# Optimization experiments

Measured on AMD Instinct MI355X. Metric: run time of the kernel, lower is better.

Reference implementation:

```python
import jax, jax.numpy as jnp
import numpy as np

D_MODEL = 1024
NUM_HEADS = 16

def setup_inputs() -> dict:
    key = jax.random.key(0)
    ks = jax.random.split(key, 5)
    std = np.sqrt(2.0 / (D_MODEL + D_MODEL))
    def w(k):
        # trunc_normal approx: normal clipped to +-3 std
        v = jax.random.truncated_normal(k, -3.0, 3.0, (D_MODEL, D_MODEL), dtype=jnp.float32) * std
        return v
    return {
        "x": jax.random.normal(ks[0], (2, 2048, D_MODEL), dtype=jnp.float32),
        "w_q": w(ks[1]),
        "w_k": w(ks[2]),
        "w_v": w(ks[3]),
        "w_o": w(ks[4]),
    }

def reference(x, w_q, w_k, w_v, w_o):
    B, S, D = x.shape
    H = NUM_HEADS
    dk = D // H
    # Linear: y = x @ W^T  (weight is [d_out, d_in])
    def proj(w):
        y = jnp.einsum('bsd,ed->bse', x, w)
        return y.reshape(B, S, H, dk).transpose(0, 2, 1, 3)  # [B,H,S,dk]
    q, k, v = proj(w_q), proj(w_k), proj(w_v)
    scale = 1.0 / jnp.sqrt(jnp.float32(dk))
    scores = jnp.einsum('bhqd,bhkd->bhqk', q, k) * scale  # [B,H,S,S]
    causal = jnp.tril(jnp.ones((S, S), dtype=bool))
    scores = jnp.where(causal, scores, -jnp.inf)
    attn = jax.nn.softmax(scores, axis=-1)
    out = jnp.einsum('bhqk,bhkd->bhqd', attn, v)  # [B,H,S,dk]
    out = out.transpose(0, 2, 1, 3).reshape(B, S, D)
    return jnp.einsum('bsd,ed->bse', out, w_o)
```

## Files before the change

### kernel.cpp

```cpp
#include <hip/hip_runtime.h>
#include <hip/hip_bf16.h>
#include <stdint.h>

#define S_LEN 2048
#define DM    1024
#define NH    16
#define DK    64
#define NBATCH 2

typedef __attribute__((ext_vector_type(8))) short bf8_t;
typedef __attribute__((ext_vector_type(4))) short s4_t;
typedef __attribute__((ext_vector_type(4))) float f4_t;

using bf16 = __hip_bfloat16;

#define NEG_BIG (-1.0e30f)
#define SCALE2  (0.125f * 1.44269504088896f)

static __device__ __forceinline__ f4_t mfma16(bf8_t a, bf8_t b, f4_t c) {
    return __builtin_amdgcn_mfma_f32_16x16x32_bf16(a, b, c, 0, 0, 0);
}

static __device__ __forceinline__ short f2b(float f) {
    __hip_bfloat16 h = __float2bfloat16(f);
    return *reinterpret_cast<short*>(&h);
}

static __device__ __forceinline__ void g2l16(const bf16* g, bf16* l) {
#if __has_builtin(__builtin_amdgcn_global_load_lds)
    __builtin_amdgcn_global_load_lds(
        (const __attribute__((address_space(1))) void*)g,
        (__attribute__((address_space(3))) void*)l, 16, 0, 0);
#else
    *(bf8_t*)l = *(const bf8_t*)g;
#endif
}

__global__ __launch_bounds__(256)
void cvt_all(const float* __restrict__ x,  const float* __restrict__ wq,
             const float* __restrict__ wk, const float* __restrict__ wv,
             const float* __restrict__ wo, bf16* __restrict__ ob) {
    const size_t SEG = 1u << 20;
    size_t i = ((size_t)blockIdx.x * 256 + threadIdx.x) * 8;
    const float* src;
    if      (i < 4 * SEG) src = x  + i;
    else if (i < 5 * SEG) src = wq + (i - 4 * SEG);
    else if (i < 6 * SEG) src = wk + (i - 5 * SEG);
    else if (i < 7 * SEG) src = wv + (i - 6 * SEG);
    else                  src = wo + (i - 7 * SEG);
    float4 f0 = *(const float4*)(src);
    float4 f1 = *(const float4*)(src + 4);
    bf8_t v;
    v[0]=f2b(f0.x); v[1]=f2b(f0.y); v[2]=f2b(f0.z); v[3]=f2b(f0.w);
    v[4]=f2b(f1.x); v[5]=f2b(f1.y); v[6]=f2b(f1.z); v[7]=f2b(f1.w);
    *(bf8_t*)(ob + i) = v;
}

#define GEMM_B_MAINLOOP(Aptr, Bptr)                                          \
    __shared__ bf16 As[128][32];                                             \
    __shared__ bf16 Bs[128][32];                                             \
    const int tid  = threadIdx.x;                                            \
    const int lane = tid & 63;                                               \
    const int w    = tid >> 6;                                               \
    const int wr   = w >> 1, wc = w & 1;                                     \
    const int lhi  = lane >> 4, llo = lane & 15;                             \
    const int bm   = blockIdx.x * 128;                                       \
    const int bn   = blockIdx.y * 128;                                       \
    const int r0c  = tid >> 2;                           \
    const int c0c  = (tid & 3) << 3;                     \
    const int r1c  = (256 + tid) >> 2;                                       \
    f4_t acc[4][4] = {};                                                     \
    for (int k0 = 0; k0 < 1024; k0 += 32) {                                  \
        __syncthreads();                                                     \
        g2l16(Aptr + (size_t)(bm + r0c) * 1024 + k0 + c0c,                   \
              &As[0][0] + (size_t)tid * 8);                                  \
        g2l16(Aptr + (size_t)(bm + r1c) * 1024 + k0 + c0c,                   \
              &As[0][0] + (size_t)(256 + tid) * 8);                          \
        g2l16(Bptr + (size_t)(bn + r0c) * 1024 + k0 + c0c,                   \
              &Bs[0][0] + (size_t)tid * 8);                                  \
        g2l16(Bptr + (size_t)(bn + r1c) * 1024 + k0 + c0c,                   \
              &Bs[0][0] + (size_t)(256 + tid) * 8);                          \
        asm volatile("s_waitcnt vmcnt(0)" ::: "memory");                     \
        __syncthreads();                                                     \
        bf8_t af[4], bfr[4];                                                 \
        _Pragma("unroll")                                                    \
        for (int i = 0; i < 4; ++i) {                                        \
            af[i]  = *(const bf8_t*)(&As[wr * 64 + i * 16 + llo][lhi * 8]);  \
            bfr[i] = *(const bf8_t*)(&Bs[wc * 64 + i * 16 + llo][lhi * 8]);  \
        }                                                                    \
        _Pragma("unroll")                                                    \
        for (int mi = 0; mi < 4; ++mi)                                       \
            _Pragma("unroll")                                                \
            for (int ni = 0; ni < 4; ++ni)                                   \
                acc[mi][ni] = mfma16(af[mi], bfr[ni], acc[mi][ni]);          \
    }

__global__ __launch_bounds__(256)
void gemm_qkv_b(const bf16* __restrict__ xb,
                const bf16* __restrict__ wqb, const bf16* __restrict__ wkb,
                const bf16* __restrict__ wvb,
                bf16* __restrict__ qws, bf16* __restrict__ kws,
                bf16* __restrict__ vtws) {
    const int z = blockIdx.z;
    const bf16* Wb = (z == 0) ? wqb : (z == 1) ? wkb : wvb;
    GEMM_B_MAINLOOP(xb, Wb)

    if (z < 2) {
        bf16* C = z ? kws : qws;
        const float sc = z ? 1.0f : SCALE2;
        #pragma unroll
        for (int mi = 0; mi < 4; ++mi)
            #pragma unroll
            for (int ni = 0; ni < 4; ++ni)
                #pragma unroll
                for (int r = 0; r < 4; ++r) {
                    int m = bm + wr * 64 + mi * 16 + lhi * 4 + r;
                    int n = bn + wc * 64 + ni * 16 + llo;
                    int b = m >> 11, s = m & (S_LEN - 1);
                    int h = n >> 6,  d = n & (DK - 1);
                    C[(((size_t)(b * NH + h) * S_LEN) + s) * DK + d] =
                        __float2bfloat16(acc[mi][ni][r] * sc);
                }
    } else {
        #pragma unroll
        for (int mi = 0; mi < 4; ++mi)
            #pragma unroll
            for (int ni = 0; ni < 4; ++ni) {
                int m0 = bm + wr * 64 + mi * 16 + lhi * 4;
                int n  = bn + wc * 64 + ni * 16 + llo;
                int b = m0 >> 11, s0 = m0 & (S_LEN - 1);
                int h = n >> 6,   d  = n & (DK - 1);
                s4_t pk;
                #pragma unroll
                for (int r = 0; r < 4; ++r) pk[r] = f2b(acc[mi][ni][r]);
                *(s4_t*)&vtws[(((size_t)(b * NH + h) * DK) + d) * S_LEN + s0] = pk;
            }
    }
}

__global__ __launch_bounds__(256)
void gemm_o_b(const bf16* __restrict__ A, const bf16* __restrict__ Wb,
              float* __restrict__ C) {
    GEMM_B_MAINLOOP(A, Wb)
    #pragma unroll
    for (int mi = 0; mi < 4; ++mi)
        #pragma unroll
        for (int ni = 0; ni < 4; ++ni)
            #pragma unroll
            for (int r = 0; r < 4; ++r) {
                int m = bm + wr * 64 + mi * 16 + lhi * 4 + r;
                int n = bn + wc * 64 + ni * 16 + llo;
                C[(size_t)m * DM + n] = acc[mi][ni][r];
            }
}

__global__ __launch_bounds__(256)
void gemm_qkv_f32(const float* __restrict__ x,
                  const float* __restrict__ wqp, const float* __restrict__ wkp,
                  const float* __restrict__ wvp,
                  bf16* __restrict__ qws, bf16* __restrict__ kws,
                  bf16* __restrict__ vtws) {
    constexpr int K = DM;
    constexpr int BM = 128, BK = 32, LDT = BK + 8;
    const int z = blockIdx.z;
    const float* W = (z == 0) ? wqp : (z == 1) ? wkp : wvp;
    __shared__ bf16 As[BM][LDT];
    __shared__ bf16 Bs[BM][LDT];
    const int tid  = threadIdx.x;
    const int lane = tid & 63;
    const int w    = tid >> 6;
    const int wr   = w >> 1, wc = w & 1;
    const int lhi  = lane >> 4, llo = lane & 15;
    const int bm   = blockIdx.x * BM;
    const int bn   = blockIdx.y * BM;
    f4_t acc[4][4] = {};
    for (int k0 = 0; k0 < K; k0 += BK) {
        __syncthreads();
        #pragma unroll
        for (int t = 0; t < 2; ++t) {
            int c   = t * 256 + tid;
            int row = c >> 2;
            int col = (c & 3) << 3;
            {
                const float* s0 = x + (size_t)(bm + row) * K + k0 + col;
                float4 f0 = *(const float4*)(s0);
                float4 f1 = *(const float4*)(s0 + 4);
                bf8_t a8;
                a8[0]=f2b(f0.x); a8[1]=f2b(f0.y); a8[2]=f2b(f0.z); a8[3]=f2b(f0.w);
                a8[4]=f2b(f1.x); a8[5]=f2b(f1.y); a8[6]=f2b(f1.z); a8[7]=f2b(f1.w);
                *(bf8_t*)(&As[row][col]) = a8;
            }
            {
                const float* s0 = W + (size_t)(bn + row) * K + k0 + col;
                float4 f0 = *(const float4*)(s0);
                float4 f1 = *(const float4*)(s0 + 4);
                bf8_t b8;
                b8[0]=f2b(f0.x); b8[1]=f2b(f0.y); b8[2]=f2b(f0.z); b8[3]=f2b(f0.w);
                b8[4]=f2b(f1.x); b8[5]=f2b(f1.y); b8[6]=f2b(f1.z); b8[7]=f2b(f1.w);
                *(bf8_t*)(&Bs[row][col]) = b8;
            }
        }
        __syncthreads();
        bf8_t af[4], bfr[4];
        #pragma unroll
        for (int i = 0; i < 4; ++i) {
            af[i]  = *(const bf8_t*)(&As[wr * 64 + i * 16 + llo][lhi * 8]);
            bfr[i] = *(const bf8_t*)(&Bs[wc * 64 + i * 16 + llo][lhi * 8]);
        }
        #pragma unroll
        for (int mi = 0; mi < 4; ++mi)
            #pragma unroll
            for (int ni = 0; ni < 4; ++ni)
                acc[mi][ni] = mfma16(af[mi], bfr[ni], acc[mi][ni]);
    }
    if (z < 2) {
        bf16* C = z ? kws : qws;
        const float sc = z ? 1.0f : SCALE2;
        #pragma unroll
        for (int mi = 0; mi < 4; ++mi)
            #pragma unroll
            for (int ni = 0; ni < 4; ++ni)
                #pragma unroll
                for (int r = 0; r < 4; ++r) {
                    int m = bm + wr * 64 + mi * 16 + lhi * 4 + r;
                    int n = bn + wc * 64 + ni * 16 + llo;
                    int b = m >> 11, s = m & (S_LEN - 1);
                    int h = n >> 6,  d = n & (DK - 1);
                    C[(((size_t)(b * NH + h) * S_LEN) + s) * DK + d] =
                        __float2bfloat16(acc[mi][ni][r] * sc);
                }
    } else {
        #pragma unroll
        for (int mi = 0; mi < 4; ++mi)
            #pragma unroll
            for (int ni = 0; ni < 4; ++ni) {
                int m0 = bm + wr * 64 + mi * 16 + lhi * 4;
                int n  = bn + wc * 64 + ni * 16 + llo;
                int b = m0 >> 11, s0 = m0 & (S_LEN - 1);
                int h = n >> 6,   d  = n & (DK - 1);
                s4_t pk;
                #pragma unroll
                for (int r = 0; r < 4; ++r) pk[r] = f2b(acc[mi][ni][r]);
                *(s4_t*)&vtws[(((size_t)(b * NH + h) * DK) + d) * S_LEN + s0] = pk;
            }
    }
}

__global__ __launch_bounds__(256)
void gemm_o_f32(const bf16* __restrict__ A, const float* __restrict__ W,
                float* __restrict__ C) {
    constexpr int N = DM;
    constexpr int K = DM;
    constexpr int BM = 128, BN = 64, BK = 32, LDT = BK + 8;
    __shared__ bf16 As[BM][LDT];
    __shared__ bf16 Bs[BN][LDT];
    const int tid  = threadIdx.x;
    const int lane = tid & 63;
    const int w    = tid >> 6;
    const int wr   = w >> 1, wc = w & 1;
    const int lhi  = lane >> 4, llo = lane & 15;
    const int bm   = blockIdx.x * BM;
    const int bn   = blockIdx.y * BN;
    f4_t acc[4][2] = {};
    for (int k0 = 0; k0 < K; k0 += BK) {
        __syncthreads();
        #pragma unroll
        for (int t = 0; t < 2; ++t) {
            int c   = t * 256 + tid;
            int row = c >> 2;
            int col = (c & 3) << 3;
            *(bf8_t*)(&As[row][col]) =
                *(const bf8_t*)(A + (size_t)(bm + row) * K + k0 + col);
        }
        {
            int row = tid >> 2;
            int col = (tid & 3) << 3;
            const float* s0 = W + (size_t)(bn + row) * K + k0 + col;
            float4 f0 = *(const float4*)(s0);
            float4 f1 = *(const float4*)(s0 + 4);
            bf8_t b8;
            b8[0]=f2b(f0.x); b8[1]=f2b(f0.y); b8[2]=f2b(f0.z); b8[3]=f2b(f0.w);
            b8[4]=f2b(f1.x); b8[5]=f2b(f1.y); b8[6]=f2b(f1.z); b8[7]=f2b(f1.w);
            *(bf8_t*)(&Bs[row][col]) = b8;
        }
        __syncthreads();
        bf8_t af[4], bfr[2];
        #pragma unroll
        for (int i = 0; i < 4; ++i)
            af[i] = *(const bf8_t*)(&As[wr * 64 + i * 16 + llo][lhi * 8]);
        #pragma unroll
        for (int i = 0; i < 2; ++i)
            bfr[i] = *(const bf8_t*)(&Bs[wc * 32 + i * 16 + llo][lhi * 8]);
        #pragma unroll
        for (int mi = 0; mi < 4; ++mi)
            #pragma unroll
            for (int ni = 0; ni < 2; ++ni)
                acc[mi][ni] = mfma16(af[mi], bfr[ni], acc[mi][ni]);
    }
    #pragma unroll
    for (int mi = 0; mi < 4; ++mi)
        #pragma unroll
        for (int ni = 0; ni < 2; ++ni)
            #pragma unroll
            for (int r = 0; r < 4; ++r) {
                int m = bm + wr * 64 + mi * 16 + lhi * 4 + r;
                int n = bn + wc * 32 + ni * 16 + llo;
                C[(size_t)m * N + n] = acc[mi][ni][r];
            }
}

__global__ __launch_bounds__(512, 4)
void attn_fwd(const bf16* __restrict__ Q, const bf16* __restrict__ K,
              const bf16* __restrict__ Vt, bf16* __restrict__ AO) {
    __shared__ bf16 Ks[2][64][64];
    __shared__ bf16 Vs[2][64][64];
    __shared__ bf16 Pl[8][16][72];

    const int bh = blockIdx.x;
    const int qt = 15 - (int)blockIdx.y;
    const int q0 = qt * 128;
    const int nt = 2 * qt + 2;

    const bf16* Qh = Q  + (size_t)bh * S_LEN * DK;
    const bf16* Kh = K  + (size_t)bh * S_LEN * DK;
    const bf16* Vh = Vt + (size_t)bh * DK * S_LEN;

    const int tid  = threadIdx.x;
    const int lane = tid & 63;
    const int w    = tid >> 6;
    const int lhi  = lane >> 4, llo = lane & 15;
    const int qw   = q0 + w * 16;
    const int sw   = llo & 7;

    const int srow = tid >> 3;
    const int schk = (tid & 7) ^ (srow & 7);

    const bf16* qrow = Qh + (size_t)(q0 + w * 16 + llo) * DK;
    const bf8_t qf0 = *(const bf8_t*)(qrow + lhi * 8);
    const bf8_t qf1 = *(const bf8_t*)(qrow + 32 + lhi * 8);

    bf8_t ones;
    #pragma unroll
    for (int j = 0; j < 8; ++j) ones[j] = (short)0x3F80;

    g2l16(Kh + (size_t)srow * DK + schk * 8, &Ks[0][0][0] + (size_t)tid * 8);
    g2l16(Vh + (size_t)srow * S_LEN + schk * 8, &Vs[0][0][0] + (size_t)tid * 8);
    asm volatile("s_waitcnt vmcnt(0)" ::: "memory");
    __syncthreads();

    f4_t o[4] = {};
    float lr[4] = {0.f, 0.f, 0.f, 0.f};
    float mr = NEG_BIG;

    for (int t = 0; t < nt; ++t) {
        const int kv0 = t * 64;
        const int cur = t & 1;

        if (t + 1 < nt) {
            g2l16(Kh + (size_t)(kv0 + 64 + srow) * DK + schk * 8,
                  &Ks[cur ^ 1][0][0] + (size_t)tid * 8);
            g2l16(Vh + (size_t)srow * S_LEN + kv0 + 64 + schk * 8,
                  &Vs[cur ^ 1][0][0] + (size_t)tid * 8);
        }

        if (kv0 <= qw + 15) {
            f4_t s[4] = {};
            __builtin_amdgcn_s_setprio(1);
            #pragma unroll
            for (int nf = 0; nf < 4; ++nf) {
                const int R = nf * 16 + llo;
                bf8_t k0f = *(const bf8_t*)&Ks[cur][R][(lhi ^ sw) * 8];
                bf8_t k1f = *(const bf8_t*)&Ks[cur][R][((4 + lhi) ^ sw) * 8];
                s[nf] = mfma16(k0f, qf0, s[nf]);
                s[nf] = mfma16(k1f, qf1, s[nf]);
            }
            __builtin_amdgcn_s_setprio(0);

            if (kv0 + 63 > qw) {
                #pragma unroll
                for (int nf = 0; nf < 4; ++nf)
                    #pragma unroll
                    for (int r = 0; r < 4; ++r)
                        if (kv0 + nf * 16 + lhi * 4 + r > qw + llo)
                            s[nf][r] = NEG_BIG;
            }

            float pm = s[0][0];
            #pragma unroll
            for (int nf = 0; nf < 4; ++nf)
                #pragma unroll
                for (int r = 0; r < 4; ++r) pm = fmaxf(pm, s[nf][r]);
            pm = fmaxf(pm, __shfl_xor(pm, 16));
            pm = fmaxf(pm, __shfl_xor(pm, 32));

            float mn = fmaxf(mr, pm);
            float alpha = exp2f(mr - mn);
            mr = mn;

            #pragma unroll
            for (int nf = 0; nf < 4; ++nf) {
                s4_t pk;
                #pragma unroll
                for (int r = 0; r < 4; ++r) pk[r] = f2b(exp2f(s[nf][r] - mr));
                *(s4_t*)&Pl[w][llo][nf * 16 + lhi * 4] = pk;
            }

            float alpha_o[4];
            #pragma unroll
            for (int r = 0; r < 4; ++r) alpha_o[r] = __shfl(alpha, lhi * 4 + r);
            #pragma unroll
            for (int df = 0; df < 4; ++df)
                #pragma unroll
                for (int r = 0; r < 4; ++r) o[df][r] *= alpha_o[r];

            asm volatile("s_waitcnt lgkmcnt(0)" ::: "memory");
            __builtin_amdgcn_sched_barrier(0);

            bf8_t pa0 = *(const bf8_t*)&Pl[w][llo][lhi * 8];
            bf8_t pa1 = *(const bf8_t*)&Pl[w][llo][32 + lhi * 8];

            f4_t rsacc = {};
            rsacc = mfma16(pa0, ones, rsacc);
            rsacc = mfma16(pa1, ones, rsacc);

            __builtin_amdgcn_s_setprio(1);
            #pragma unroll
            for (int df = 0; df < 4; ++df) {
                const int R = df * 16 + llo;
                bf8_t vb0 = *(const bf8_t*)&Vs[cur][R][(lhi ^ sw) * 8];
                bf8_t vb1 = *(const bf8_t*)&Vs[cur][R][((4 + lhi) ^ sw) * 8];
                o[df] = mfma16(pa0, vb0, o[df]);
                o[df] = mfma16(pa1, vb1, o[df]);
            }
            __builtin_amdgcn_s_setprio(0);

            #pragma unroll
            for (int r = 0; r < 4; ++r) lr[r] = lr[r] * alpha_o[r] + rsacc[r];
        }

        asm volatile("s_waitcnt vmcnt(0)" ::: "memory");
        __syncthreads();
    }

    const int b = bh >> 4, h = bh & (NH - 1);
    #pragma unroll
    for (int r = 0; r < 4; ++r) {
        float inv = 1.0f / lr[r];
        int q = q0 + w * 16 + lhi * 4 + r;
        bf16* orow = AO + ((size_t)(b * S_LEN + q) * DM) + h * DK;
        #pragma unroll
        for (int df = 0; df < 4; ++df)
            orow[df * 16 + llo] = __float2bfloat16(o[df][r] * inv);
    }
}

extern "C" void kernel_launch(void* const* d_in, const int* in_sizes, int n_in,
                              void* d_out, int out_size, void* d_ws, size_t ws_size,
                              hipStream_t stream) {
    const float* x  = (const float*)d_in[0];
    const float* wq = (const float*)d_in[1];
    const float* wk = (const float*)d_in[2];
    const float* wv = (const float*)d_in[3];
    const float* wo = (const float*)d_in[4];
    float* out = (float*)d_out;

    const size_t SEG   = 1u << 20;
    const size_t elems = 4 * SEG;
    const size_t need_fast = (8 * SEG + 3 * elems) * sizeof(bf16);

    dim3 blk(256);

    if (ws_size >= need_fast) {
        bf16* ob   = (bf16*)d_ws;
        bf16* xb   = ob;
        bf16* wqb  = ob + 4 * SEG;
        bf16* wkb  = ob + 5 * SEG;
        bf16* wvb  = ob + 6 * SEG;
        bf16* wob  = ob + 7 * SEG;
        bf16* qws  = ob + 8 * SEG;
        bf16* kws  = qws + elems;
        bf16* vtws = kws + elems;
        bf16* aws  = xb;

        cvt_all<<<4096, blk, 0, stream>>>(x, wq, wk, wv, wo, ob);
        gemm_qkv_b<<<dim3(32, 8, 3), blk, 0, stream>>>(xb, wqb, wkb, wvb,
                                                       qws, kws, vtws);
        attn_fwd<<<dim3(NBATCH * NH, 16), dim3(512), 0, stream>>>(qws, kws, vtws, aws);
        gemm_o_b<<<dim3(32, 8), blk, 0, stream>>>(aws, wob, out);
    } else {
        if (ws_size < elems * 4 * sizeof(bf16)) return;
        bf16* qws  = (bf16*)d_ws;
        bf16* kws  = qws + elems;
        bf16* vtws = kws + elems;
        bf16* aws  = vtws + elems;

        gemm_qkv_f32<<<dim3(32, 8, 3), blk, 0, stream>>>(x, wq, wk, wv,
                                                         qws, kws, vtws);
        attn_fwd<<<dim3(NBATCH * NH, 16), dim3(512), 0, stream>>>(qws, kws, vtws, aws);
        gemm_o_f32<<<dim3(32, 16), blk, 0, stream>>>(aws, wo, out);
    }
}
```

Baseline: 120.8 us.

## Triple-buffer attention KV, lazy rescaling, remap grid, smaller output GEMM tiles

```diff
diff --git a/kernel.cpp b/kernel.cpp
--- a/kernel.cpp
+++ b/kernel.cpp
@@ -141,15 +141,50 @@
 __global__ __launch_bounds__(256)
 void gemm_o_b(const bf16* __restrict__ A, const bf16* __restrict__ Wb,
               float* __restrict__ C) {
-    GEMM_B_MAINLOOP(A, Wb)
+    __shared__ bf16 As[128][32];
+    __shared__ bf16 Bs[64][32];
+    const int tid  = threadIdx.x;
+    const int lane = tid & 63;
+    const int w    = tid >> 6;
+    const int wr   = w >> 1, wc = w & 1;
+    const int lhi  = lane >> 4, llo = lane & 15;
+    const int bm   = blockIdx.x * 128;
+    const int bn   = blockIdx.y * 64;
+    const int r0c  = tid >> 2;
+    const int c0c  = (tid & 3) << 3;
+    const int r1c  = (256 + tid) >> 2;
+    f4_t acc[4][2] = {};
+    for (int k0 = 0; k0 < 1024; k0 += 32) {
+        __syncthreads();
+        g2l16(A + (size_t)(bm + r0c) * 1024 + k0 + c0c,
+              &As[0][0] + (size_t)tid * 8);
+        g2l16(A + (size_t)(bm + r1c) * 1024 + k0 + c0c,
+              &As[0][0] + (size_t)(256 + tid) * 8);
+        g2l16(Wb + (size_t)(bn + r0c) * 1024 + k0 + c0c,
+              &Bs[0][0] + (size_t)tid * 8);
+        asm volatile("s_waitcnt vmcnt(0)" ::: "memory");
+        __syncthreads();
+        bf8_t af[4], bfr[2];
+        #pragma unroll
+        for (int i = 0; i < 4; ++i)
+            af[i] = *(const bf8_t*)(&As[wr * 64 + i * 16 + llo][lhi * 8]);
+        #pragma unroll
+        for (int i = 0; i < 2; ++i)
+            bfr[i] = *(const bf8_t*)(&Bs[wc * 32 + i * 16 + llo][lhi * 8]);
+        #pragma unroll
+        for (int mi = 0; mi < 4; ++mi)
+            #pragma unroll
+            for (int ni = 0; ni < 2; ++ni)
+                acc[mi][ni] = mfma16(af[mi], bfr[ni], acc[mi][ni]);
+    }
     #pragma unroll
     for (int mi = 0; mi < 4; ++mi)
         #pragma unroll
-        for (int ni = 0; ni < 4; ++ni)
+        for (int ni = 0; ni < 2; ++ni)
             #pragma unroll
             for (int r = 0; r < 4; ++r) {
                 int m = bm + wr * 64 + mi * 16 + lhi * 4 + r;
-                int n = bn + wc * 64 + ni * 16 + llo;
+                int n = bn + wc * 32 + ni * 16 + llo;
                 C[(size_t)m * DM + n] = acc[mi][ni][r];
             }
 }
@@ -312,12 +347,13 @@
 __global__ __launch_bounds__(512, 4)
 void attn_fwd(const bf16* __restrict__ Q, const bf16* __restrict__ K,
               const bf16* __restrict__ Vt, bf16* __restrict__ AO) {
-    __shared__ bf16 Ks[2][64][64];
-    __shared__ bf16 Vs[2][64][64];
+    __shared__ bf16 Ks[3][64][64];
+    __shared__ bf16 Vs[3][64][64];
     __shared__ bf16 Pl[8][16][72];
 
-    const int bh = blockIdx.x;
-    const int qt = 15 - (int)blockIdx.y;
+    const int l  = ((int)blockIdx.x & 7) * 64 + ((int)blockIdx.x >> 3);
+    const int bh = l >> 4;
+    const int qt = 15 - (l & 15);
     const int q0 = qt * 128;
     const int nt = 2 * qt + 2;
 
@@ -335,6 +371,14 @@
     const int srow = tid >> 3;
     const int schk = (tid & 7) ^ (srow & 7);
 
+#define STAGE(kv, b)                                                          \
+    do {                                                                      \
+        g2l16(Kh + (size_t)((kv) + srow) * DK + schk * 8,                     \
+              &Ks[b][0][0] + (size_t)tid * 8);                                \
+        g2l16(Vh + (size_t)srow * S_LEN + (kv) + schk * 8,                    \
+              &Vs[b][0][0] + (size_t)tid * 8);                                \
+    } while (0)
+
     const bf16* qrow = Qh + (size_t)(q0 + w * 16 + llo) * DK;
     const bf8_t qf0 = *(const bf8_t*)(qrow + lhi * 8);
     const bf8_t qf1 = *(const bf8_t*)(qrow + 32 + lhi * 8);
@@ -343,10 +387,10 @@
     #pragma unroll
     for (int j = 0; j < 8; ++j) ones[j] = (short)0x3F80;
 
-    g2l16(Kh + (size_t)srow * DK + schk * 8, &Ks[0][0][0] + (size_t)tid * 8);
-    g2l16(Vh + (size_t)srow * S_LEN + schk * 8, &Vs[0][0][0] + (size_t)tid * 8);
-    asm volatile("s_waitcnt vmcnt(0)" ::: "memory");
-    __syncthreads();
+    STAGE(0, 0);
+    STAGE(64, 1);
+    asm volatile("s_waitcnt vmcnt(2)" ::: "memory");
+    __builtin_amdgcn_s_barrier();
 
     f4_t o[4] = {};
     float lr[4] = {0.f, 0.f, 0.f, 0.f};
@@ -354,14 +398,9 @@
 
     for (int t = 0; t < nt; ++t) {
         const int kv0 = t * 64;
-        const int cur = t & 1;
-
-        if (t + 1 < nt) {
-            g2l16(Kh + (size_t)(kv0 + 64 + srow) * DK + schk * 8,
-                  &Ks[cur ^ 1][0][0] + (size_t)tid * 8);
-            g2l16(Vh + (size_t)srow * S_LEN + kv0 + 64 + schk * 8,
-                  &Vs[cur ^ 1][0][0] + (size_t)tid * 8);
-        }
+        const int cur = t % 3;
+        const bool more = (t + 2 < nt);
+        if (more) STAGE((t + 2) * 64, (t + 2) % 3);
 
         if (kv0 <= qw + 15) {
             f4_t s[4] = {};
@@ -393,9 +432,20 @@
             pm = fmaxf(pm, __shfl_xor(pm, 16));
             pm = fmaxf(pm, __shfl_xor(pm, 32));
 
-            float mn = fmaxf(mr, pm);
-            float alpha = exp2f(mr - mn);
-            mr = mn;
+            if (__any(pm > mr + 8.0f)) {
+                float mn = fmaxf(mr, pm);
+                float alpha = exp2f(mr - mn);
+                mr = mn;
+                float ao[4];
+                #pragma unroll
+                for (int r = 0; r < 4; ++r) ao[r] = __shfl(alpha, lhi * 4 + r);
+                #pragma unroll
+                for (int df = 0; df < 4; ++df)
+                    #pragma unroll
+                    for (int r = 0; r < 4; ++r) o[df][r] *= ao[r];
+                #pragma unroll
+                for (int r = 0; r < 4; ++r) lr[r] *= ao[r];
+            }
 
             #pragma unroll
             for (int nf = 0; nf < 4; ++nf) {
@@ -404,14 +454,6 @@
                 for (int r = 0; r < 4; ++r) pk[r] = f2b(exp2f(s[nf][r] - mr));
                 *(s4_t*)&Pl[w][llo][nf * 16 + lhi * 4] = pk;
             }
-
-            float alpha_o[4];
-            #pragma unroll
-            for (int r = 0; r < 4; ++r) alpha_o[r] = __shfl(alpha, lhi * 4 + r);
-            #pragma unroll
-            for (int df = 0; df < 4; ++df)
-                #pragma unroll
-                for (int r = 0; r < 4; ++r) o[df][r] *= alpha_o[r];
 
             asm volatile("s_waitcnt lgkmcnt(0)" ::: "memory");
             __builtin_amdgcn_sched_barrier(0);
@@ -435,12 +477,14 @@
             __builtin_amdgcn_s_setprio(0);
 
             #pragma unroll
-            for (int r = 0; r < 4; ++r) lr[r] = lr[r] * alpha_o[r] + rsacc[r];
+            for (int r = 0; r < 4; ++r) lr[r] += rsacc[r];
         }
 
-        asm volatile("s_waitcnt vmcnt(0)" ::: "memory");
-        __syncthreads();
-    }
+        if (more) asm volatile("s_waitcnt vmcnt(2)" ::: "memory");
+        else      asm volatile("s_waitcnt vmcnt(0)" ::: "memory");
+        __builtin_amdgcn_s_barrier();
+    }
+#undef STAGE
 
     const int b = bh >> 4, h = bh & (NH - 1);
     #pragma unroll
@@ -485,8 +529,8 @@
         cvt_all<<<4096, blk, 0, stream>>>(x, wq, wk, wv, wo, ob);
         gemm_qkv_b<<<dim3(32, 8, 3), blk, 0, stream>>>(xb, wqb, wkb, wvb,
                                                        qws, kws, vtws);
-        attn_fwd<<<dim3(NBATCH * NH, 16), dim3(512), 0, stream>>>(qws, kws, vtws, aws);
-        gemm_o_b<<<dim3(32, 8), blk, 0, stream>>>(aws, wob, out);
+        attn_fwd<<<dim3(512), dim3(512), 0, stream>>>(qws, kws, vtws, aws);
+        gemm_o_b<<<dim3(32, 16), blk, 0, stream>>>(aws, wob, out);
     } else {
         if (ws_size < elems * 4 * sizeof(bf16)) return;
         bf16* qws  = (bf16*)d_ws;
@@ -496,7 +540,7 @@
 
         gemm_qkv_f32<<<dim3(32, 8, 3), blk, 0, stream>>>(x, wq, wk, wv,
                                                          qws, kws, vtws);
-        attn_fwd<<<dim3(NBATCH * NH, 16), dim3(512), 0, stream>>>(qws, kws, vtws, aws);
+        attn_fwd<<<dim3(512), dim3(512), 0, stream>>>(qws, kws, vtws, aws);
         gemm_o_f32<<<dim3(32, 16), blk, 0, stream>>>(aws, wo, out);
     }
 }
```

New measurement: 129.3 us. 1.07x slower.
